# Kernel optimization log

Hardware: AMD Instinct MI355X
Metric: run time of the kernel (lower is better)

The kernel has to match this reference:

```python
import jax, jax.numpy as jnp
import numpy as np

N, E, IN_DIM, HID = 50000, 800000, 128, 256
H2 = HID // 2
LN_EPS = 1e-5


def setup_inputs() -> dict:
    key = jax.random.key(0)
    ks = jax.random.split(key, 20)
    s = lambda k, shape, fan: jax.random.normal(k, shape, jnp.float32) * (1.0 / np.sqrt(fan))
    return {
        "x": jax.random.normal(ks[0], (N, IN_DIM), jnp.float32),
        "edge_index": jax.random.randint(ks[1], (2, E), 0, N, jnp.int64),
        # GATConv(in_dim, H2, heads=1, concat=False)
        "W_gat": s(ks[2], (IN_DIM, H2), IN_DIM),
        "att_src": s(ks[3], (H2,), H2),
        "att_dst": s(ks[4], (H2,), H2),
        "b_gat": jnp.zeros((H2,), jnp.float32),
        # SAGEConv(in_dim, H2): lin_l (with bias) on aggregated, lin_r (no bias) on root
        "W1l": s(ks[5], (IN_DIM, H2), IN_DIM),
        "b1l": jnp.zeros((H2,), jnp.float32),
        "W1r": s(ks[6], (IN_DIM, H2), IN_DIM),
        "ln1_g": jnp.ones((HID,), jnp.float32),
        "ln1_b": jnp.zeros((HID,), jnp.float32),
        # SAGEConv(hidden, hidden)
        "W2l": s(ks[7], (HID, HID), HID),
        "b2l": jnp.zeros((HID,), jnp.float32),
        "W2r": s(ks[8], (HID, HID), HID),
        "ln2_g": jnp.ones((HID,), jnp.float32),
        "ln2_b": jnp.zeros((HID,), jnp.float32),
        "Wc": s(ks[9], (HID, 1), HID),
        "bc": jnp.zeros((1,), jnp.float32),
    }


def _layernorm(h, g, b):
    mu = jnp.mean(h, axis=-1, keepdims=True)
    var = jnp.mean(jnp.square(h - mu), axis=-1, keepdims=True)
    return (h - mu) * jax.lax.rsqrt(var + LN_EPS) * g + b


def _sage(x, src, dst, Wl, bl, Wr, n):
    # mean aggregation of source features at destination, then lin_l(agg) + lin_r(x)
    s = jax.ops.segment_sum(x[src], dst, num_segments=n)
    deg = jax.ops.segment_sum(jnp.ones((src.shape[0],), x.dtype), dst, num_segments=n)
    agg = s / jnp.maximum(deg, 1.0)[:, None]
    return agg @ Wl + bl + x @ Wr


def _gat(x, src, dst, W, a_s, a_d, b, n):
    # heads=1, concat=False, add_self_loops=True, eval (no dropout)
    loop = jnp.arange(n)
    gs = jnp.concatenate([src, loop])
    gd = jnp.concatenate([dst, loop])
    h = x @ W                                  # [N, H2]
    e = jax.nn.leaky_relu(jnp.take(h @ a_s, gs) + jnp.take(h @ a_d, gd), 0.2)
    emax = jax.ops.segment_max(e, gd, num_segments=n)
    ex = jnp.exp(e - emax[gd])
    denom = jax.ops.segment_sum(ex, gd, num_segments=n)
    alpha = ex / denom[gd]                     # scatter-softmax over in-edges
    out = jax.ops.segment_sum(alpha[:, None] * h[gs], gd, num_segments=n)
    return out + b


def reference(x, edge_index, W_gat, att_src, att_dst, b_gat,
              W1l, b1l, W1r, ln1_g, ln1_b,
              W2l, b2l, W2r, ln2_g, ln2_b, Wc, bc):
    n = x.shape[0]
    src, dst = edge_index[0], edge_index[1]
    x1 = _gat(x, src, dst, W_gat, att_src, att_dst, b_gat, n)
    x2 = _sage(x, src, dst, W1l, b1l, W1r, n)
    h = jnp.concatenate([x1, x2], axis=-1)
    h = jax.nn.relu(_layernorm(h, ln1_g, ln1_b))
    h = _sage(h, src, dst, W2l, b2l, W2r, n)
    h = jax.nn.relu(_layernorm(h, ln2_g, ln2_b))
    return (h @ Wc + bc).squeeze(-1)
```

## Files before the change

kernel.cpp:

```cpp
#include <hip/hip_runtime.h>

#define LN_EPS 1e-5f
#define CA 4096
#define CAPB 6144

typedef __attribute__((ext_vector_type(8))) short short8;
typedef __attribute__((ext_vector_type(4))) float float4a;
typedef __attribute__((ext_vector_type(2))) float float2a;

__device__ __forceinline__ float lrelu(float v) { return v > 0.f ? v : 0.2f * v; }

__device__ __forceinline__ unsigned short f2bf(float f) {
    union { float f; unsigned int u; } x; x.f = f;
    unsigned int u = x.u;
    unsigned int r = (u + 0x7fffu + ((u >> 16) & 1u)) >> 16;
    return (unsigned short)r;
}
__device__ __forceinline__ float bflo(unsigned int v) {
    union { unsigned int u; float f; } x; x.u = v << 16; return x.f;
}
__device__ __forceinline__ float bfhi(unsigned int v) {
    union { unsigned int u; float f; } x; x.u = v & 0xffff0000u; return x.f;
}
__device__ __forceinline__ float2a bf2(unsigned int w) {
    union { unsigned int u; float f; } lo, hi;
    lo.u = w << 16; hi.u = w & 0xffff0000u;
    float2a r; r[0] = lo.f; r[1] = hi.f; return r;
}

__device__ __forceinline__ void load_lds16(const void* g, void* l) {
    __builtin_amdgcn_global_load_lds(
        (const __attribute__((address_space(1))) void*)g,
        (__attribute__((address_space(3))) void*)l, 16, 0, 0);
}

__device__ __forceinline__ void accb(float2a aw2[4], float2a ap2[4], float w, uint4 v) {
    float2a wm2; wm2[0] = w; wm2[1] = w;
    float2a f0 = bf2(v.x), f1 = bf2(v.y), f2v = bf2(v.z), f3 = bf2(v.w);
    aw2[0] += wm2 * f0; aw2[1] += wm2 * f1;
    aw2[2] += wm2 * f2v; aw2[3] += wm2 * f3;
    ap2[0] += f0; ap2[1] += f1;
    ap2[2] += f2v; ap2[3] += f3;
}

__device__ __forceinline__ void accbm(float2a aw2[4], float2a ap2[4], float wm, float sm, uint4 v) {
    float2a wm2; wm2[0] = wm; wm2[1] = wm;
    float2a sm2; sm2[0] = sm; sm2[1] = sm;
    float2a f0 = bf2(v.x), f1 = bf2(v.y), f2v = bf2(v.z), f3 = bf2(v.w);
    aw2[0] += wm2 * f0; aw2[1] += wm2 * f1;
    aw2[2] += wm2 * f2v; aw2[3] += wm2 * f3;
    ap2[0] += sm2 * f0; ap2[1] += sm2 * f1;
    ap2[2] += sm2 * f2v; ap2[3] += sm2 * f3;
}

__global__ void prep(const float* __restrict__ W_gat, const float* __restrict__ W1l,
                     const float* __restrict__ W1r, const float* __restrict__ W2l,
                     const float* __restrict__ W2r,
                     const float* __restrict__ att_s, const float* __restrict__ att_d,
                     unsigned short* __restrict__ W12T, unsigned short* __restrict__ W2cT,
                     float* __restrict__ vs, float* __restrict__ vd)
{
    int idx = blockIdx.x * 256 + threadIdx.x;
    if (idx < 98304) {
        int c = idx / 384, k = idx - c * 384;
        float v = 0.f;
        if (c < 128) { if (k < 128) v = W_gat[k * 128 + c]; }
        else {
            int cc = c - 128;
            if (k >= 256)       v = W1r[(k - 256) * 128 + cc];
            else if (k >= 128)  v = W1l[(k - 128) * 128 + cc];
        }
        W12T[idx] = f2bf(v);
    } else if (idx < 229376) {
        int t = idx - 98304;
        int c = t >> 9, k = t & 511;
        float v = (k < 256) ? W2l[k * 256 + c] : W2r[(k - 256) * 256 + c];
        W2cT[t] = f2bf(v);
    } else if (idx < 229376 + 128) {
        int k = idx - 229376;
        float s = 0.f, d = 0.f;
        for (int c = 0; c < 128; ++c) {
            float w = W_gat[k * 128 + c];
            s += w * att_s[c]; d += w * att_d[c];
        }
        vs[k] = s; vd[k] = d;
    }
}

__global__ __launch_bounds__(256) void conv_x_asad(
    const float* __restrict__ x, const float* __restrict__ vs, const float* __restrict__ vd,
    unsigned short* __restrict__ combo3, float* __restrict__ as_, float* __restrict__ ad_, int N)
{
    const int wave = threadIdx.x >> 6, lane = threadIdx.x & 63;
    const int i = blockIdx.x * 4 + wave;
    if (i >= N) return;
    float2 xv = *(const float2*)(x + (size_t)i * 128 + 2 * lane);
    float2 vsv = *(const float2*)(vs + 2 * lane);
    float2 vdv = *(const float2*)(vd + 2 * lane);
    float s = xv.x * vsv.x + xv.y * vsv.y;
    float d = xv.x * vdv.x + xv.y * vdv.y;
    #pragma unroll
    for (int off = 32; off > 0; off >>= 1) {
        s += __shfl_xor(s, off);
        d += __shfl_xor(d, off);
    }
    if (lane == 0) { as_[i] = s; ad_[i] = d; }
    unsigned pk = (unsigned)f2bf(xv.x) | ((unsigned)f2bf(xv.y) << 16);
    *(unsigned*)(combo3 + (size_t)i * 384 + 256 + 2 * lane) = pk;
}

__global__ __launch_bounds__(256) void radix_hist(
    const int* __restrict__ dst, int E, int* __restrict__ blockhist, int B)
{
    const int blk = blockIdx.x, t = threadIdx.x;
    __shared__ int hist[256];
    hist[t] = 0; __syncthreads();
    const int chunk = blk * CA, cend = min(chunk + CA, E);
    for (int j = chunk + t; j < cend; j += 256)
        atomicAdd(&hist[((unsigned)dst[j]) >> 8], 1);
    __syncthreads();
    blockhist[t * B + blk] = hist[t];
}

__global__ __launch_bounds__(256) void scan_rows(
    int* __restrict__ blockhist, int B, int* __restrict__ bintot)
{
    const int bin = blockIdx.x, t = threadIdx.x;
    __shared__ int tmp[256];
    __shared__ int carry;
    if (t == 0) carry = 0;
    __syncthreads();
    const int base = bin * B;
    for (int off0 = 0; off0 < B; off0 += 256) {
        int i = off0 + t;
        int v = (i < B) ? blockhist[base + i] : 0;
        tmp[t] = v; __syncthreads();
        for (int off = 1; off < 256; off <<= 1) {
            int a = (t >= off) ? tmp[t - off] : 0;
            __syncthreads();
            tmp[t] += a;
            __syncthreads();
        }
        int incl = tmp[t] + carry;
        if (i < B) blockhist[base + i] = incl - v;
        __syncthreads();
        if (t == 255) carry = incl;
        __syncthreads();
    }
    if (t == 0) bintot[bin] = carry;
}

__global__ __launch_bounds__(256) void scan_bins(
    const int* __restrict__ bintot, int* __restrict__ bucket_base, int E)
{
    const int t = threadIdx.x;
    __shared__ int tmp[256];
    int v = bintot[t];
    tmp[t] = v; __syncthreads();
    for (int off = 1; off < 256; off <<= 1) {
        int a = (t >= off) ? tmp[t - off] : 0;
        __syncthreads();
        tmp[t] += a;
        __syncthreads();
    }
    bucket_base[t] = tmp[t] - v;
    if (t == 255) bucket_base[256] = E;
}

__global__ __launch_bounds__(256) void radix_scatter(
    const int* __restrict__ src, const int* __restrict__ dst, int E,
    const int* __restrict__ rowscan, const int* __restrict__ bucket_base,
    int B, unsigned int* __restrict__ srt)
{
    const int blk = blockIdx.x, t = threadIdx.x;
    __shared__ int hist[256], lscan[256], lcur[256], gbase[256];
    __shared__ unsigned int recs[CA];
    hist[t] = 0; __syncthreads();
    const int chunk = blk * CA, cend = min(chunk + CA, E);
    for (int j = chunk + t; j < cend; j += 256)
        atomicAdd(&hist[((unsigned)dst[j]) >> 8], 1);
    __syncthreads();
    lscan[t] = hist[t]; __syncthreads();
    for (int off = 1; off < 256; off <<= 1) {
        int a = (t >= off) ? lscan[t - off] : 0;
        __syncthreads();
        lscan[t] += a;
        __syncthreads();
    }
    int excl = lscan[t] - hist[t];
    __syncthreads();
    lscan[t] = excl; lcur[t] = excl;
    gbase[t] = bucket_base[t] + rowscan[t * B + blk];
    __syncthreads();
    for (int j = chunk + t; j < cend; j += 256) {
        int d = dst[j];
        unsigned int r = ((unsigned)d << 16) | (unsigned)src[j];
        int p = atomicAdd(&lcur[((unsigned)d) >> 8], 1);
        recs[p] = r;
    }
    __syncthreads();
    const int cnt = cend - chunk;
    for (int k = t; k < cnt; k += 256) {
        unsigned int r = recs[k];
        int bin = r >> 24;
        srt[gbase[bin] + (k - lscan[bin])] = r;
    }
}

__global__ __launch_bounds__(256) void bucket_sort(
    const unsigned int* __restrict__ srt, const int* __restrict__ bucket_base,
    unsigned short* __restrict__ col_src, int* __restrict__ rp, int N, int E)
{
    const int b = blockIdx.x, t = threadIdx.x;
    const int beg = bucket_base[b], end = bucket_base[b + 1];
    const int cnt = end - beg;
    __shared__ int hist[256], lscan[256], lcur[256];
    __shared__ unsigned int recs[CAPB];
    __shared__ unsigned short outr[CAPB];
    hist[t] = 0; __syncthreads();
    const bool fits = cnt <= CAPB;
    if (fits) {
        for (int j = beg + t; j < end; j += 256) {
            unsigned int r = srt[j];
            recs[j - beg] = r;
            atomicAdd(&hist[(r >> 16) & 255], 1);
        }
    } else {
        for (int j = beg + t; j < end; j += 256)
            atomicAdd(&hist[(srt[j] >> 16) & 255], 1);
    }
    __syncthreads();
    lscan[t] = hist[t]; __syncthreads();
    for (int off = 1; off < 256; off <<= 1) {
        int a = (t >= off) ? lscan[t - off] : 0;
        __syncthreads();
        lscan[t] += a;
        __syncthreads();
    }
    int excl = lscan[t] - hist[t];
    __syncthreads();
    lscan[t] = excl; lcur[t] = excl;
    int d = (b << 8) + t;
    if (d < N) rp[d] = beg + excl;
    if (b == gridDim.x - 1 && t == 0) rp[N] = E;
    __syncthreads();
    if (fits) {
        for (int k = t; k < cnt; k += 256) {
            unsigned int r = recs[k];
            int p = atomicAdd(&lcur[(r >> 16) & 255], 1);
            outr[p] = (unsigned short)(r & 0xFFFFu);
        }
        __syncthreads();
        for (int k = t; k < cnt; k += 256)
            col_src[beg + k] = outr[k];
    } else {
        for (int j = beg + t; j < end; j += 256) {
            unsigned int r = srt[j];
            int p = atomicAdd(&lcur[(r >> 16) & 255], 1);
            col_src[beg + p] = (unsigned short)(r & 0xFFFFu);
        }
    }
}

__global__ __launch_bounds__(256) void gat_sage1(
    const int* __restrict__ row_ptr, const unsigned short* __restrict__ col_src,
    const float* __restrict__ as_, const float* __restrict__ ad_,
    unsigned short* __restrict__ combo3, int N)
{
    const int wave = threadIdx.x >> 6, lane = threadIdx.x & 63;
    const int i = blockIdx.x * 4 + wave;
    if (i >= N) return;
    const int g = lane >> 4, l15 = lane & 15;
    const int beg = row_ptr[i], end = row_ptr[i + 1];
    const int deg = end - beg;
    const float adi = ad_[i];
    const float wself = __expf(lrelu(as_[i] + adi));

    int j = beg + lane;
    int sn_l = (j < end) ? (int)col_src[j] : 0;
    float w_l = (j < end) ? __expf(lrelu(as_[sn_l] + adi)) : 0.f;

    const unsigned short* myp = combo3 + 256 + 8 * l15;

    uint4 sv = *(const uint4*)(myp + (size_t)i * 384);
    const int dc = deg < 64 ? deg : 64;
    const int nr = dc >> 3;
    uint4 pv0, pv1; float pw0 = 0.f, pw1 = 0.f;
    if (nr > 0) {
        int sn0 = __shfl(sn_l, g), sn1 = __shfl(sn_l, 4 + g);
        pw0 = __shfl(w_l, g); pw1 = __shfl(w_l, 4 + g);
        pv0 = *(const uint4*)(myp + (size_t)sn0 * 384);
        pv1 = *(const uint4*)(myp + (size_t)sn1 * 384);
    }

    float2a aw2[4], ap2[4];
    {
        float wm = (g == 0) ? wself : 0.f;
        float2a wm2; wm2[0] = wm; wm2[1] = wm;
        aw2[0] = wm2 * bf2(sv.x); aw2[1] = wm2 * bf2(sv.y);
        aw2[2] = wm2 * bf2(sv.z); aw2[3] = wm2 * bf2(sv.w);
        #pragma unroll
        for (int k = 0; k < 4; ++k) { ap2[k][0] = 0.f; ap2[k][1] = 0.f; }
    }

    for (int r = 0; r < nr; ++r) {
        uint4 cv0 = pv0, cv1 = pv1;
        float cw0 = pw0, cw1 = pw1;
        if (r + 1 < nr) {
            int b8 = (r + 1) * 8;
            int sn0 = __shfl(sn_l, b8 + g), sn1 = __shfl(sn_l, b8 + 4 + g);
            pw0 = __shfl(w_l, b8 + g); pw1 = __shfl(w_l, b8 + 4 + g);
            pv0 = *(const uint4*)(myp + (size_t)sn0 * 384);
            pv1 = *(const uint4*)(myp + (size_t)sn1 * 384);
        }
        accb(aw2, ap2, cw0, cv0);
        accb(aw2, ap2, cw1, cv1);
    }
    for (int j2 = nr * 8; j2 < dc; j2 += 4) {
        int eidx = j2 + g;
        bool val = eidx < dc;
        int sn  = __shfl(sn_l, val ? eidx : 0);
        float w = __shfl(w_l, val ? eidx : 0);
        uint4 v = *(const uint4*)(myp + (size_t)sn * 384);
        accbm(aw2, ap2, val ? w : 0.f, val ? 1.f : 0.f, v);
    }
    for (int j3 = 64; j3 < deg; ++j3) {
        int sn = col_src[beg + j3];
        float w = __expf(lrelu(as_[sn] + adi));
        uint4 v = *(const uint4*)(myp + (size_t)sn * 384);
        accbm(aw2, ap2, (g == 0) ? w : 0.f, (g == 0) ? 1.f : 0.f, v);
    }

    float s = w_l;
    for (int jj = beg + lane + 64; jj < end; jj += 64)
        s += __expf(lrelu(as_[col_src[jj]] + adi));
    #pragma unroll
    for (int off = 32; off > 0; off >>= 1) s += __shfl_xor(s, off);
    const float denom = s + wself;

    float aw[8], ap[8];
    #pragma unroll
    for (int k = 0; k < 4; ++k) {
        aw[2 * k] = aw2[k][0]; aw[2 * k + 1] = aw2[k][1];
        ap[2 * k] = ap2[k][0]; ap[2 * k + 1] = ap2[k][1];
    }
    #pragma unroll
    for (int k = 0; k < 8; ++k) {
        aw[k] += __shfl_xor(aw[k], 16); aw[k] += __shfl_xor(aw[k], 32);
        ap[k] += __shfl_xor(ap[k], 16); ap[k] += __shfl_xor(ap[k], 32);
    }
    if (g == 0) {
        float inv = 1.f / denom;
        uint4 pk;
        pk.x = (unsigned)f2bf(aw[0] * inv) | ((unsigned)f2bf(aw[1] * inv) << 16);
        pk.y = (unsigned)f2bf(aw[2] * inv) | ((unsigned)f2bf(aw[3] * inv) << 16);
        pk.z = (unsigned)f2bf(aw[4] * inv) | ((unsigned)f2bf(aw[5] * inv) << 16);
        pk.w = (unsigned)f2bf(aw[6] * inv) | ((unsigned)f2bf(aw[7] * inv) << 16);
        *(uint4*)(combo3 + (size_t)i * 384 + 8 * l15) = pk;
    } else if (g == 1) {
        float dinv = 1.f / fmaxf((float)deg, 1.f);
        uint4 pk;
        pk.x = (unsigned)f2bf(ap[0] * dinv) | ((unsigned)f2bf(ap[1] * dinv) << 16);
        pk.y = (unsigned)f2bf(ap[2] * dinv) | ((unsigned)f2bf(ap[3] * dinv) << 16);
        pk.z = (unsigned)f2bf(ap[4] * dinv) | ((unsigned)f2bf(ap[5] * dinv) << 16);
        pk.w = (unsigned)f2bf(ap[6] * dinv) | ((unsigned)f2bf(ap[7] * dinv) << 16);
        *(uint4*)(combo3 + (size_t)i * 384 + 128 + 8 * l15) = pk;
    }
}

__device__ __forceinline__ int swz_kk(int v) {
    return (((v & 7) ^ ((v >> 3) & 7)) * 8);
}

__global__ __launch_bounds__(256) void gemm12_ln(
    const unsigned short* __restrict__ combo3, int M,
    const unsigned short* __restrict__ W12T,
    const float* __restrict__ b_gat, const float* __restrict__ b1l,
    const float* __restrict__ g1, const float* __restrict__ bb1,
    unsigned short* __restrict__ combo2, unsigned char* __restrict__ hq)
{
    __shared__ __align__(16) unsigned short As[64 * 64];
    __shared__ __align__(16) unsigned short Ws[256 * 64];
    const int tid = threadIdx.x;
    const int bm = blockIdx.x * 64;
    const int wave = tid >> 6, lane = tid & 63;
    const int quad = lane >> 4, l15 = lane & 15;
    const int swz_rd = (l15 & 7) * 8;

    float4a acc[4][4];
    const float4a z4 = {0.f, 0.f, 0.f, 0.f};
    #pragma unroll
    for (int i = 0; i < 4; ++i)
        #pragma unroll
        for (int j = 0; j < 4; ++j) acc[i][j] = z4;

    for (int k0 = 0; k0 < 384; k0 += 64) {
        #pragma unroll
        for (int it = 0; it < 2; ++it) {
            int v = tid + it * 256;
            int r = v >> 3, kk = swz_kk(v);
            if (bm + r < M)
                load_lds16(combo3 + (size_t)(bm + r) * 384 + k0 + kk, &As[v * 8]);
        }
        #pragma unroll
        for (int it = 0; it < 8; ++it) {
            int v = tid + it * 256;
            int r = v >> 3, kk = swz_kk(v);
            load_lds16(W12T + (size_t)r * 384 + k0 + kk, &Ws[v * 8]);
        }
        __syncthreads();
        #pragma unroll
        for (int ks = 0; ks < 64; ks += 32) {
            short8 af[4], bfr[4];
            #pragma unroll
            for (int i = 0; i < 4; ++i)
                af[i] = *(const short8*)(&As[(i * 16 + l15) * 64 + ((ks + quad * 8) ^ swz_rd)]);
            #pragma unroll
            for (int j = 0; j < 4; ++j)
                bfr[j] = *(const short8*)(&Ws[(wave * 64 + j * 16 + l15) * 64 + ((ks + quad * 8) ^ swz_rd)]);
            #pragma unroll
            for (int i = 0; i < 4; ++i)
                #pragma unroll
                for (int j = 0; j < 4; ++j)
                    acc[i][j] = __builtin_amdgcn_mfma_f32_16x16x32_bf16(af[i], bfr[j], acc[i][j], 0, 0, 0);
        }
        __syncthreads();
    }
    int col[4]; float bcol[4], gc[4], bc2[4];
    #pragma unroll
    for (int j = 0; j < 4; ++j) {
        int c = wave * 64 + j * 16 + l15;
        col[j] = c;
        bcol[j] = (c < 128) ? b_gat[c] : b1l[c - 128];
        gc[j] = g1[c]; bc2[j] = bb1[c];
    }
    float* lsum = (float*)As;
    float* lsq  = lsum + 256;
    #pragma unroll
    for (int i = 0; i < 4; ++i)
        #pragma unroll
        for (int r = 0; r < 4; ++r) {
            float ps = 0.f, pq = 0.f;
            #pragma unroll
            for (int j = 0; j < 4; ++j) {
                float v = acc[i][j][r] + bcol[j];
                ps += v; pq += v * v;
            }
            #pragma unroll
            for (int off = 1; off < 16; off <<= 1) {
                ps += __shfl_xor(ps, off);
                pq += __shfl_xor(pq, off);
            }
            if (l15 == 0) {
                int row = i * 16 + quad * 4 + r;
                lsum[row * 4 + wave] = ps;
                lsq[row * 4 + wave]  = pq;
            }
        }
    __syncthreads();
    unsigned short* Hs = Ws;
    #pragma unroll
    for (int i = 0; i < 4; ++i)
        #pragma unroll
        for (int r = 0; r < 4; ++r) {
            int row = i * 16 + quad * 4 + r;
            float su = lsum[row * 4] + lsum[row * 4 + 1] + lsum[row * 4 + 2] + lsum[row * 4 + 3];
            float sq = lsq[row * 4] + lsq[row * 4 + 1] + lsq[row * 4 + 2] + lsq[row * 4 + 3];
            float mu = su * (1.f / 256.f);
            float var = sq * (1.f / 256.f) - mu * mu;
            float rs = rsqrtf(var + LN_EPS);
            #pragma unroll
            for (int j = 0; j < 4; ++j) {
                float v = acc[i][j][r] + bcol[j];
                float o = fmaxf((v - mu) * rs * gc[j] + bc2[j], 0.f);
                Hs[row * 256 + col[j]] = f2bf(o);
            }
        }
    __syncthreads();
    #pragma unroll
    for (int it = 0; it < 8; ++it) {
        int v = tid + it * 256;
        int r = v >> 5, cc = (v & 31) * 8;
        if (bm + r < M)
            *(uint4*)(combo2 + (size_t)(bm + r) * 512 + 256 + cc) = *(const uint4*)(&Hs[r * 256 + cc]);
    }
    #pragma unroll
    for (int it = 0; it < 4; ++it) {
        int v = tid + it * 256;
        int r = v >> 4, c16 = (v & 15) * 16;
        if (bm + r < M) {
            uint4 o;
            #pragma unroll
            for (int q = 0; q < 4; ++q) {
                unsigned int w0 = *(const unsigned int*)(&Hs[r * 256 + c16 + q * 4 + 0]);
                unsigned int w1 = *(const unsigned int*)(&Hs[r * 256 + c16 + q * 4 + 2]);
                unsigned int t0 = __builtin_amdgcn_cvt_pk_fp8_f32(bflo(w0), bfhi(w0), 0, false);
                unsigned int t1 = __builtin_amdgcn_cvt_pk_fp8_f32(bflo(w1), bfhi(w1), t0, true);
                ((unsigned int*)&o)[q] = t1;
            }
            *(uint4*)(hq + (size_t)(bm + r) * 256 + c16) = o;
        }
    }
}

__global__ __launch_bounds__(256) void sage2_agg(
    const int* __restrict__ row_ptr, const unsigned short* __restrict__ col_src,
    const unsigned char* __restrict__ hq, unsigned short* __restrict__ combo2, int N)
{
    const int wave = threadIdx.x >> 6, lane = threadIdx.x & 63;
    const int i = blockIdx.x * 4 + wave;
    if (i >= N) return;
    const int g = lane >> 4, l15 = lane & 15;
    const int beg = row_ptr[i], end = row_ptr[i + 1];
    const int deg = end - beg;
    int cidx = (beg + lane < end) ? (int)col_src[beg + lane] : 0;
    const unsigned char* myp = hq + 16 * l15;
    float2a a2[8];
    #pragma unroll
    for (int k = 0; k < 8; ++k) { a2[k][0] = 0.f; a2[k][1] = 0.f; }
    const int dc = deg < 64 ? deg : 64;
    int j = 0;
    for (; j + 8 <= dc; j += 8) {
        #pragma unroll
        for (int u = 0; u < 2; ++u) {
            int eidx = j + 4 * u + g;
            int sn = __shfl(cidx, eidx);
            uint4 v = *(const uint4*)(myp + (size_t)sn * 256);
            a2[0] += __builtin_amdgcn_cvt_pk_f32_fp8(v.x, false);
            a2[1] += __builtin_amdgcn_cvt_pk_f32_fp8(v.x, true);
            a2[2] += __builtin_amdgcn_cvt_pk_f32_fp8(v.y, false);
            a2[3] += __builtin_amdgcn_cvt_pk_f32_fp8(v.y, true);
            a2[4] += __builtin_amdgcn_cvt_pk_f32_fp8(v.z, false);
            a2[5] += __builtin_amdgcn_cvt_pk_f32_fp8(v.z, true);
            a2[6] += __builtin_amdgcn_cvt_pk_f32_fp8(v.w, false);
            a2[7] += __builtin_amdgcn_cvt_pk_f32_fp8(v.w, true);
        }
    }
    for (; j < dc; j += 4) {
        int eidx = j + g;
        bool val = eidx < dc;
        int sn = __shfl(cidx, val ? eidx : 0);
        uint4 v = *(const uint4*)(myp + (size_t)sn * 256);
        float mlt = val ? 1.f : 0.f;
        float2a m2; m2[0] = mlt; m2[1] = mlt;
        a2[0] += m2 * __builtin_amdgcn_cvt_pk_f32_fp8(v.x, false);
        a2[1] += m2 * __builtin_amdgcn_cvt_pk_f32_fp8(v.x, true);
        a2[2] += m2 * __builtin_amdgcn_cvt_pk_f32_fp8(v.y, false);
        a2[3] += m2 * __builtin_amdgcn_cvt_pk_f32_fp8(v.y, true);
        a2[4] += m2 * __builtin_amdgcn_cvt_pk_f32_fp8(v.z, false);
        a2[5] += m2 * __builtin_amdgcn_cvt_pk_f32_fp8(v.z, true);
        a2[6] += m2 * __builtin_amdgcn_cvt_pk_f32_fp8(v.w, false);
        a2[7] += m2 * __builtin_amdgcn_cvt_pk_f32_fp8(v.w, true);
    }
    for (int j3 = 64; j3 < deg; ++j3) {
        int sn = col_src[beg + j3];
        uint4 v = *(const uint4*)(myp + (size_t)sn * 256);
        float mlt = (g == 0) ? 1.f : 0.f;
        float2a m2; m2[0] = mlt; m2[1] = mlt;
        a2[0] += m2 * __builtin_amdgcn_cvt_pk_f32_fp8(v.x, false);
        a2[1] += m2 * __builtin_amdgcn_cvt_pk_f32_fp8(v.x, true);
        a2[2] += m2 * __builtin_amdgcn_cvt_pk_f32_fp8(v.y, false);
        a2[3] += m2 * __builtin_amdgcn_cvt_pk_f32_fp8(v.y, true);
        a2[4] += m2 * __builtin_amdgcn_cvt_pk_f32_fp8(v.z, false);
        a2[5] += m2 * __builtin_amdgcn_cvt_pk_f32_fp8(v.z, true);
        a2[6] += m2 * __builtin_amdgcn_cvt_pk_f32_fp8(v.w, false);
        a2[7] += m2 * __builtin_amdgcn_cvt_pk_f32_fp8(v.w, true);
    }
    float a[16];
    #pragma unroll
    for (int k = 0; k < 8; ++k) { a[2 * k] = a2[k][0]; a[2 * k + 1] = a2[k][1]; }
    #pragma unroll
    for (int k = 0; k < 16; ++k) {
        a[k] += __shfl_xor(a[k], 16);
        a[k] += __shfl_xor(a[k], 32);
    }
    if (g == 0) {
        float dinv = 1.f / fmaxf((float)deg, 1.f);
        uint4 pk0, pk1;
        pk0.x = (unsigned)f2bf(a[0] * dinv)  | ((unsigned)f2bf(a[1] * dinv)  << 16);
        pk0.y = (unsigned)f2bf(a[2] * dinv)  | ((unsigned)f2bf(a[3] * dinv)  << 16);
        pk0.z = (unsigned)f2bf(a[4] * dinv)  | ((unsigned)f2bf(a[5] * dinv)  << 16);
        pk0.w = (unsigned)f2bf(a[6] * dinv)  | ((unsigned)f2bf(a[7] * dinv)  << 16);
        pk1.x = (unsigned)f2bf(a[8] * dinv)  | ((unsigned)f2bf(a[9] * dinv)  << 16);
        pk1.y = (unsigned)f2bf(a[10] * dinv) | ((unsigned)f2bf(a[11] * dinv) << 16);
        pk1.z = (unsigned)f2bf(a[12] * dinv) | ((unsigned)f2bf(a[13] * dinv) << 16);
        pk1.w = (unsigned)f2bf(a[14] * dinv) | ((unsigned)f2bf(a[15] * dinv) << 16);
        *(uint4*)(combo2 + (size_t)i * 512 + 16 * l15)     = pk0;
        *(uint4*)(combo2 + (size_t)i * 512 + 16 * l15 + 8) = pk1;
    }
}

__global__ __launch_bounds__(256) void gemm3_out(
    const unsigned short* __restrict__ combo2, int M,
    const unsigned short* __restrict__ W2cT,
    const float* __restrict__ b2l,
    const float* __restrict__ g2, const float* __restrict__ bb2,
    const float* __restrict__ Wc, const float* __restrict__ bc,
    float* __restrict__ out)
{
    __shared__ __align__(16) unsigned short As[64 * 64];
    __shared__ __align__(16) unsigned short Ws[256 * 64];
    const int tid = threadIdx.x;
    const int bm = blockIdx.x * 64;
    const int wave = tid >> 6, lane = tid & 63;
    const int quad = lane >> 4, l15 = lane & 15;
    const int swz_rd = (l15 & 7) * 8;

    float4a acc[4][4];
    const float4a z4 = {0.f, 0.f, 0.f, 0.f};
    #pragma unroll
    for (int i = 0; i < 4; ++i)
        #pragma unroll
        for (int j = 0; j < 4; ++j) acc[i][j] = z4;

    for (int k0 = 0; k0 < 512; k0 += 64) {
        #pragma unroll
        for (int it = 0; it < 2; ++it) {
            int v = tid + it * 256;
            int r = v >> 3, kk = swz_kk(v);
            if (bm + r < M)
                load_lds16(combo2 + (size_t)(bm + r) * 512 + k0 + kk, &As[v * 8]);
        }
        #pragma unroll
        for (int it = 0; it < 8; ++it) {
            int v = tid + it * 256;
            int r = v >> 3, kk = swz_kk(v);
            load_lds16(W2cT + (size_t)r * 512 + k0 + kk, &Ws[v * 8]);
        }
        __syncthreads();
        #pragma unroll
        for (int ks = 0; ks < 64; ks += 32) {
            short8 af[4], bfr[4];
            #pragma unroll
            for (int i = 0; i < 4; ++i)
                af[i] = *(const short8*)(&As[(i * 16 + l15) * 64 + ((ks + quad * 8) ^ swz_rd)]);
            #pragma unroll
            for (int j = 0; j < 4; ++j)
                bfr[j] = *(const short8*)(&Ws[(wave * 64 + j * 16 + l15) * 64 + ((ks + quad * 8) ^ swz_rd)]);
            #pragma unroll
            for (int i = 0; i < 4; ++i)
                #pragma unroll
                for (int j = 0; j < 4; ++j)
                    acc[i][j] = __builtin_amdgcn_mfma_f32_16x16x32_bf16(af[i], bfr[j], acc[i][j], 0, 0, 0);
        }
        __syncthreads();
    }
    int col[4]; float bcol[4], gc[4], bc2[4], wcl[4];
    #pragma unroll
    for (int j = 0; j < 4; ++j) {
        int c = wave * 64 + j * 16 + l15;
        col[j] = c;
        bcol[j] = b2l[c];
        gc[j] = g2[c]; bc2[j] = bb2[c]; wcl[j] = Wc[c];
    }
    float* lsum = (float*)As;
    float* lsq  = lsum + 256;
    float* ldot = lsum + 512;
    #pragma unroll
    for (int i = 0; i < 4; ++i)
        #pragma unroll
        for (int r = 0; r < 4; ++r) {
            float ps = 0.f, pq = 0.f;
            #pragma unroll
            for (int j = 0; j < 4; ++j) {
                float v = acc[i][j][r] + bcol[j];
                ps += v; pq += v * v;
            }
            #pragma unroll
            for (int off = 1; off < 16; off <<= 1) {
                ps += __shfl_xor(ps, off);
                pq += __shfl_xor(pq, off);
            }
            if (l15 == 0) {
                int row = i * 16 + quad * 4 + r;
                lsum[row * 4 + wave] = ps;
                lsq[row * 4 + wave]  = pq;
            }
        }
    __syncthreads();
    #pragma unroll
    for (int i = 0; i < 4; ++i)
        #pragma unroll
        for (int r = 0; r < 4; ++r) {
            int row = i * 16 + quad * 4 + r;
            float su = lsum[row * 4] + lsum[row * 4 + 1] + lsum[row * 4 + 2] + lsum[row * 4 + 3];
            float sq = lsq[row * 4] + lsq[row * 4 + 1] + lsq[row * 4 + 2] + lsq[row * 4 + 3];
            float mu = su * (1.f / 256.f);
            float var = sq * (1.f / 256.f) - mu * mu;
            float rs = rsqrtf(var + LN_EPS);
            float pd = 0.f;
            #pragma unroll
            for (int j = 0; j < 4; ++j) {
                float v = acc[i][j][r] + bcol[j];
                float o = fmaxf((v - mu) * rs * gc[j] + bc2[j], 0.f);
                pd += o * wcl[j];
            }
            #pragma unroll
            for (int off = 1; off < 16; off <<= 1) pd += __shfl_xor(pd, off);
            if (l15 == 0) ldot[row * 4 + wave] = pd;
        }
    __syncthreads();
    if (tid < 64 && bm + tid < M)
        out[bm + tid] = ldot[tid * 4] + ldot[tid * 4 + 1] + ldot[tid * 4 + 2] + ldot[tid * 4 + 3] + bc[0];
}

extern "C" void kernel_launch(void* const* d_in, const int* in_sizes, int n_in,
                              void* d_out, int out_size, void* d_ws, size_t ws_size,
                              hipStream_t stream)
{
    const float* x     = (const float*)d_in[0];
    const int*   ei    = (const int*)d_in[1];
    const float* W_gat = (const float*)d_in[2];
    const float* att_s = (const float*)d_in[3];
    const float* att_d = (const float*)d_in[4];
    const float* b_gat = (const float*)d_in[5];
    const float* W1l   = (const float*)d_in[6];
    const float* b1l   = (const float*)d_in[7];
    const float* W1r   = (const float*)d_in[8];
    const float* ln1g  = (const float*)d_in[9];
    const float* ln1b  = (const float*)d_in[10];
    const float* W2l   = (const float*)d_in[11];
    const float* b2l   = (const float*)d_in[12];
    const float* W2r   = (const float*)d_in[13];
    const float* ln2g  = (const float*)d_in[14];
    const float* ln2b  = (const float*)d_in[15];
    const float* Wc    = (const float*)d_in[16];
    const float* bc    = (const float*)d_in[17];

    const int N = in_sizes[0] / 128;
    const int E = in_sizes[1] / 2;
    const int* srcp = ei;
    const int* dstp = ei + E;

    char* p = (char*)d_ws;
    unsigned short* combo3 = (unsigned short*)p; p += (size_t)N * 384 * 2;
    unsigned short* combo2 = (unsigned short*)p; p += (size_t)N * 512 * 2;
    unsigned char* hq     = (unsigned char*)p;  p += (size_t)N * 256;
    float* as_    = (float*)p;                 p += (size_t)N * 4;
    float* ad_    = (float*)p;                 p += (size_t)N * 4;
    float* vs     = (float*)p;                 p += 128 * 4;
    float* vd     = (float*)p;                 p += 128 * 4;
    unsigned short* W12T = (unsigned short*)p; p += (size_t)256 * 384 * 2;
    unsigned short* W2cT = (unsigned short*)p; p += (size_t)256 * 512 * 2;
    unsigned int* srt    = (unsigned int*)p;   p += (size_t)E * 4;
    unsigned short* col_src = (unsigned short*)p; p += (((size_t)E * 2 + 15) & ~15ull);
    int* rp       = (int*)p;                   p += (size_t)(N + 1) * 4;
    const int B   = (E + CA - 1) / CA;
    int* blockhist = (int*)p;                  p += (size_t)256 * B * 4;
    int* bucket_base = (int*)p;                p += 257 * 4;
    int* bintot   = (int*)p;                   p += 256 * 4;

    dim3 b256(256);
    const int mb64 = (N + 63) / 64;
    const int nb = (N + 255) >> 8;
    const int prep_total = 229376 + 128;

    hipLaunchKernelGGL(prep, dim3((prep_total + 255) / 256), b256, 0, stream,
                       W_gat, W1l, W1r, W2l, W2r, att_s, att_d, W12T, W2cT, vs, vd);
    hipLaunchKernelGGL(conv_x_asad, dim3((N + 3) / 4), b256, 0, stream,
                       x, vs, vd, combo3, as_, ad_, N);

    hipLaunchKernelGGL(radix_hist, dim3(B), b256, 0, stream, dstp, E, blockhist, B);
    hipLaunchKernelGGL(scan_rows, dim3(256), b256, 0, stream, blockhist, B, bintot);
    hipLaunchKernelGGL(scan_bins, dim3(1), b256, 0, stream, bintot, bucket_base, E);
    hipLaunchKernelGGL(radix_scatter, dim3(B), b256, 0, stream,
                       srcp, dstp, E, blockhist, bucket_base, B, srt);
    hipLaunchKernelGGL(bucket_sort, dim3(nb), b256, 0, stream,
                       srt, bucket_base, col_src, rp, N, E);

    hipLaunchKernelGGL(gat_sage1, dim3((N + 3) / 4), b256, 0, stream,
                       rp, col_src, as_, ad_, combo3, N);

    hipLaunchKernelGGL(gemm12_ln, dim3(mb64), b256, 0, stream,
                       combo3, N, W12T, b_gat, b1l, ln1g, ln1b, combo2, hq);

    hipLaunchKernelGGL(sage2_agg, dim3((N + 3) / 4), b256, 0, stream,
                       rp, col_src, hq, combo2, N);

    hipLaunchKernelGGL(gemm3_out, dim3(mb64), b256, 0, stream,
                       combo2, N, W2cT, b2l, ln2g, ln2b, Wc, bc, (float*)d_out);
}
```

Baseline: 280.0 us.

## Replace two-pass radix sort CSR build with atomic degree count and scatter

```diff
diff --git a/kernel.cpp b/kernel.cpp
--- a/kernel.cpp
+++ b/kernel.cpp
@@ -1,8 +1,6 @@
 #include <hip/hip_runtime.h>
 
 #define LN_EPS 1e-5f
-#define CA 4096
-#define CAPB 6144
 
 typedef __attribute__((ext_vector_type(8))) short short8;
 typedef __attribute__((ext_vector_type(4))) float float4a;
@@ -109,31 +107,44 @@
     *(unsigned*)(combo3 + (size_t)i * 384 + 256 + 2 * lane) = pk;
 }
 
-__global__ __launch_bounds__(256) void radix_hist(
-    const int* __restrict__ dst, int E, int* __restrict__ blockhist, int B)
-{
-    const int blk = blockIdx.x, t = threadIdx.x;
-    __shared__ int hist[256];
-    hist[t] = 0; __syncthreads();
-    const int chunk = blk * CA, cend = min(chunk + CA, E);
-    for (int j = chunk + t; j < cend; j += 256)
-        atomicAdd(&hist[((unsigned)dst[j]) >> 8], 1);
-    __syncthreads();
-    blockhist[t * B + blk] = hist[t];
-}
-
-__global__ __launch_bounds__(256) void scan_rows(
-    int* __restrict__ blockhist, int B, int* __restrict__ bintot)
-{
-    const int bin = blockIdx.x, t = threadIdx.x;
+__global__ __launch_bounds__(256) void deg_hist(
+    const int* __restrict__ dst, int E, int* __restrict__ deg)
+{
+    int j = blockIdx.x * 256 + threadIdx.x;
+    const int stride = gridDim.x * 256;
+    for (; j < E; j += stride)
+        atomicAdd(&deg[dst[j]], 1);
+}
+
+__global__ __launch_bounds__(256) void scan_local(
+    const int* __restrict__ deg, int N, int* __restrict__ texcl, int* __restrict__ btot)
+{
+    const int b = blockIdx.x, t = threadIdx.x;
+    const int i = b * 256 + t;
+    __shared__ int tmp[256];
+    int v = (i < N) ? deg[i] : 0;
+    tmp[t] = v; __syncthreads();
+    for (int off = 1; off < 256; off <<= 1) {
+        int a = (t >= off) ? tmp[t - off] : 0;
+        __syncthreads();
+        tmp[t] += a;
+        __syncthreads();
+    }
+    if (i < N) texcl[i] = tmp[t] - v;
+    if (t == 255) btot[b] = tmp[255];
+}
+
+__global__ __launch_bounds__(256) void scan_blocks(
+    const int* __restrict__ btot, int* __restrict__ bbase, int B)
+{
+    const int t = threadIdx.x;
     __shared__ int tmp[256];
     __shared__ int carry;
     if (t == 0) carry = 0;
     __syncthreads();
-    const int base = bin * B;
-    for (int off0 = 0; off0 < B; off0 += 256) {
-        int i = off0 + t;
-        int v = (i < B) ? blockhist[base + i] : 0;
+    for (int o = 0; o < B; o += 256) {
+        int i = o + t;
+        int v = (i < B) ? btot[i] : 0;
         tmp[t] = v; __syncthreads();
         for (int off = 1; off < 256; off <<= 1) {
             int a = (t >= off) ? tmp[t - off] : 0;
@@ -141,124 +152,35 @@
             tmp[t] += a;
             __syncthreads();
         }
-        int incl = tmp[t] + carry;
-        if (i < B) blockhist[base + i] = incl - v;
+        if (i < B) bbase[i] = tmp[t] - v + carry;
         __syncthreads();
-        if (t == 255) carry = incl;
+        if (t == 255) carry += tmp[255];
         __syncthreads();
     }
-    if (t == 0) bintot[bin] = carry;
-}
-
-__global__ __launch_bounds__(256) void scan_bins(
-    const int* __restrict__ bintot, int* __restrict__ bucket_base, int E)
-{
-    const int t = threadIdx.x;
-    __shared__ int tmp[256];
-    int v = bintot[t];
-    tmp[t] = v; __syncthreads();
-    for (int off = 1; off < 256; off <<= 1) {
-        int a = (t >= off) ? tmp[t - off] : 0;
-        __syncthreads();
-        tmp[t] += a;
-        __syncthreads();
-    }
-    bucket_base[t] = tmp[t] - v;
-    if (t == 255) bucket_base[256] = E;
-}
-
-__global__ __launch_bounds__(256) void radix_scatter(
+}
+
+__global__ __launch_bounds__(256) void finalize_rp(
+    const int* __restrict__ texcl, const int* __restrict__ bbase,
+    int N, int E, int* __restrict__ rp, int* __restrict__ cur)
+{
+    const int i = blockIdx.x * 256 + threadIdx.x;
+    if (i < N) {
+        int v = texcl[i] + bbase[blockIdx.x];
+        rp[i] = v; cur[i] = v;
+    }
+    if (i == 0) rp[N] = E;
+}
+
+__global__ __launch_bounds__(256) void scatter_edges(
     const int* __restrict__ src, const int* __restrict__ dst, int E,
-    const int* __restrict__ rowscan, const int* __restrict__ bucket_base,
-    int B, unsigned int* __restrict__ srt)
-{
-    const int blk = blockIdx.x, t = threadIdx.x;
-    __shared__ int hist[256], lscan[256], lcur[256], gbase[256];
-    __shared__ unsigned int recs[CA];
-    hist[t] = 0; __syncthreads();
-    const int chunk = blk * CA, cend = min(chunk + CA, E);
-    for (int j = chunk + t; j < cend; j += 256)
-        atomicAdd(&hist[((unsigned)dst[j]) >> 8], 1);
-    __syncthreads();
-    lscan[t] = hist[t]; __syncthreads();
-    for (int off = 1; off < 256; off <<= 1) {
-        int a = (t >= off) ? lscan[t - off] : 0;
-        __syncthreads();
-        lscan[t] += a;
-        __syncthreads();
-    }
-    int excl = lscan[t] - hist[t];
-    __syncthreads();
-    lscan[t] = excl; lcur[t] = excl;
-    gbase[t] = bucket_base[t] + rowscan[t * B + blk];
-    __syncthreads();
-    for (int j = chunk + t; j < cend; j += 256) {
+    int* __restrict__ cur, unsigned short* __restrict__ col_src)
+{
+    int j = blockIdx.x * 256 + threadIdx.x;
+    const int stride = gridDim.x * 256;
+    for (; j < E; j += stride) {
         int d = dst[j];
-        unsigned int r = ((unsigned)d << 16) | (unsigned)src[j];
-        int p = atomicAdd(&lcur[((unsigned)d) >> 8], 1);
-        recs[p] = r;
-    }
-    __syncthreads();
-    const int cnt = cend - chunk;
-    for (int k = t; k < cnt; k += 256) {
-        unsigned int r = recs[k];
-        int bin = r >> 24;
-        srt[gbase[bin] + (k - lscan[bin])] = r;
-    }
-}
-
-__global__ __launch_bounds__(256) void bucket_sort(
-    const unsigned int* __restrict__ srt, const int* __restrict__ bucket_base,
-    unsigned short* __restrict__ col_src, int* __restrict__ rp, int N, int E)
-{
-    const int b = blockIdx.x, t = threadIdx.x;
-    const int beg = bucket_base[b], end = bucket_base[b + 1];
-    const int cnt = end - beg;
-    __shared__ int hist[256], lscan[256], lcur[256];
-    __shared__ unsigned int recs[CAPB];
-    __shared__ unsigned short outr[CAPB];
-    hist[t] = 0; __syncthreads();
-    const bool fits = cnt <= CAPB;
-    if (fits) {
-        for (int j = beg + t; j < end; j += 256) {
-            unsigned int r = srt[j];
-            recs[j - beg] = r;
-            atomicAdd(&hist[(r >> 16) & 255], 1);
-        }
-    } else {
-        for (int j = beg + t; j < end; j += 256)
-            atomicAdd(&hist[(srt[j] >> 16) & 255], 1);
-    }
-    __syncthreads();
-    lscan[t] = hist[t]; __syncthreads();
-    for (int off = 1; off < 256; off <<= 1) {
-        int a = (t >= off) ? lscan[t - off] : 0;
-        __syncthreads();
-        lscan[t] += a;
-        __syncthreads();
-    }
-    int excl = lscan[t] - hist[t];
-    __syncthreads();
-    lscan[t] = excl; lcur[t] = excl;
-    int d = (b << 8) + t;
-    if (d < N) rp[d] = beg + excl;
-    if (b == gridDim.x - 1 && t == 0) rp[N] = E;
-    __syncthreads();
-    if (fits) {
-        for (int k = t; k < cnt; k += 256) {
-            unsigned int r = recs[k];
-            int p = atomicAdd(&lcur[(r >> 16) & 255], 1);
-            outr[p] = (unsigned short)(r & 0xFFFFu);
-        }
-        __syncthreads();
-        for (int k = t; k < cnt; k += 256)
-            col_src[beg + k] = outr[k];
-    } else {
-        for (int j = beg + t; j < end; j += 256) {
-            unsigned int r = srt[j];
-            int p = atomicAdd(&lcur[(r >> 16) & 255], 1);
-            col_src[beg + p] = (unsigned short)(r & 0xFFFFu);
-        }
+        int p = atomicAdd(&cur[d], 1);
+        col_src[p] = (unsigned short)src[j];
     }
 }
 
@@ -742,17 +664,17 @@
     float* vd     = (float*)p;                 p += 128 * 4;
     unsigned short* W12T = (unsigned short*)p; p += (size_t)256 * 384 * 2;
     unsigned short* W2cT = (unsigned short*)p; p += (size_t)256 * 512 * 2;
-    unsigned int* srt    = (unsigned int*)p;   p += (size_t)E * 4;
     unsigned short* col_src = (unsigned short*)p; p += (((size_t)E * 2 + 15) & ~15ull);
     int* rp       = (int*)p;                   p += (size_t)(N + 1) * 4;
-    const int B   = (E + CA - 1) / CA;
-    int* blockhist = (int*)p;                  p += (size_t)256 * B * 4;
-    int* bucket_base = (int*)p;                p += 257 * 4;
-    int* bintot   = (int*)p;                   p += 256 * 4;
+    int* deg      = (int*)p;                   p += (size_t)N * 4;
+    int* texcl    = (int*)p;                   p += (size_t)N * 4;
+    int* cur      = (int*)p;                   p += (size_t)N * 4;
+    const int SB  = (N + 255) >> 8;
+    int* btot     = (int*)p;                   p += (size_t)SB * 4;
+    int* bbase    = (int*)p;                   p += (size_t)SB * 4;
 
     dim3 b256(256);
     const int mb64 = (N + 63) / 64;
-    const int nb = (N + 255) >> 8;
     const int prep_total = 229376 + 128;
 
     hipLaunchKernelGGL(prep, dim3((prep_total + 255) / 256), b256, 0, stream,
@@ -760,13 +682,12 @@
     hipLaunchKernelGGL(conv_x_asad, dim3((N + 3) / 4), b256, 0, stream,
                        x, vs, vd, combo3, as_, ad_, N);
 
-    hipLaunchKernelGGL(radix_hist, dim3(B), b256, 0, stream, dstp, E, blockhist, B);
-    hipLaunchKernelGGL(scan_rows, dim3(256), b256, 0, stream, blockhist, B, bintot);
-    hipLaunchKernelGGL(scan_bins, dim3(1), b256, 0, stream, bintot, bucket_base, E);
-    hipLaunchKernelGGL(radix_scatter, dim3(B), b256, 0, stream,
-                       srcp, dstp, E, blockhist, bucket_base, B, srt);
-    hipLaunchKernelGGL(bucket_sort, dim3(nb), b256, 0, stream,
-                       srt, bucket_base, col_src, rp, N, E);
+    hipMemsetAsync(deg, 0, (size_t)N * 4, stream);
+    hipLaunchKernelGGL(deg_hist, dim3(1024), b256, 0, stream, dstp, E, deg);
+    hipLaunchKernelGGL(scan_local, dim3(SB), b256, 0, stream, deg, N, texcl, btot);
+    hipLaunchKernelGGL(scan_blocks, dim3(1), b256, 0, stream, btot, bbase, SB);
+    hipLaunchKernelGGL(finalize_rp, dim3(SB), b256, 0, stream, texcl, bbase, N, E, rp, cur);
+    hipLaunchKernelGGL(scatter_edges, dim3(1024), b256, 0, stream, srcp, dstp, E, cur, col_src);
 
     hipLaunchKernelGGL(gat_sage1, dim3((N + 3) / 4), b256, 0, stream,
                        rp, col_src, as_, ad_, combo3, N);
```

Result: slower. 348.1 us (+24.3%).
